# Kernel optimization log

Hardware: AMD Instinct MI355X
Metric: run time of the kernel (lower is better)

The kernel has to match this reference:

```python
import jax, jax.numpy as jnp
import numpy as np

EPS = 1e-5


def setup_inputs() -> dict:
    key = jax.random.key(0)
    k_x, k_y, k_w, k_b = jax.random.split(key, 4)
    B, IN, OUT = 16384, 1024, 1024
    x = jax.random.normal(k_x, (B, IN), dtype=jnp.float32)
    y = jax.random.normal(k_y, (B, OUT), dtype=jnp.float32)
    # nn.Linear default init scale ~ 1/sqrt(in_features); keep activations sane
    weight = jax.random.normal(k_w, (OUT, IN), dtype=jnp.float32) / np.sqrt(IN)
    bias = jax.random.normal(k_b, (OUT,), dtype=jnp.float32) / np.sqrt(IN)
    gamma = jnp.ones((OUT,), dtype=jnp.float32)
    beta = jnp.zeros((OUT,), dtype=jnp.float32)
    return {"x": x, "y": y, "weight": weight, "bias": bias, "gamma": gamma, "beta": beta}


def reference(x, y, weight, bias, gamma, beta):
    # Linear: z[b, o] = sum_i x[b, i] * weight[o, i] + bias[o]
    z = jnp.einsum('bi,oi->bo', x, weight) + bias
    # LayerNorm over the feature (out_features) dim, biased variance
    mean = jnp.mean(z, axis=-1, keepdims=True)
    var = jnp.mean(jnp.square(z), axis=-1, keepdims=True) - jnp.square(mean)
    ln = (z - mean) * jax.lax.rsqrt(var + EPS) * gamma + beta
    # residual add then elementwise multiply
    return (ln + y) * y
```

## Files before the change

kernel.cpp:

```cpp
#include <hip/hip_runtime.h>
#include <stdint.h>

typedef unsigned short u16;
typedef __attribute__((ext_vector_type(8))) short short8;
typedef __attribute__((ext_vector_type(4))) float floatx4;
typedef __attribute__((ext_vector_type(2))) float floatx2;

#define K_DIM 1024
#define N_DIM 1024
#define BM 64
#define BK 32
#define NCHUNK (K_DIM / BK)

__device__ __forceinline__ u16 f2b(float f) {
    union { float f; uint32_t i; } v; v.f = f;
    uint32_t u = v.i;
    return (u16)((u + 0x7FFFu + ((u >> 16) & 1u)) >> 16);
}
__device__ __forceinline__ float b2f(u16 u) {
    union { uint32_t i; float f; } v; v.i = ((uint32_t)u) << 16; return v.f;
}

__global__ __launch_bounds__(256) void pack_w_kernel(const float* __restrict__ w,
                                                     u16* __restrict__ wpk) {
    int gid  = blockIdx.x * 256 + threadIdx.x;
    int lane = gid & 63;
    int kc   = (gid >> 6) & 31;
    int tile = gid >> 11;
    int n = tile * 16 + (lane & 15);
    int k = kc * 32 + (lane >> 4) * 8;
    const float* src = w + (size_t)n * K_DIM + k;
    floatx4 a = *(const floatx4*)(src);
    floatx4 b = *(const floatx4*)(src + 4);
    short8 o;
    o[0] = (short)f2b(a[0]); o[1] = (short)f2b(a[1]);
    o[2] = (short)f2b(a[2]); o[3] = (short)f2b(a[3]);
    o[4] = (short)f2b(b[0]); o[5] = (short)f2b(b[1]);
    o[6] = (short)f2b(b[2]); o[7] = (short)f2b(b[3]);
    *(short8*)(wpk + (size_t)gid * 8) = o;
}

__global__ __launch_bounds__(1024) void fused_gemm_ln_kernel(
    const float* __restrict__ x, const float* __restrict__ y,
    const u16* __restrict__ wpk, const float* __restrict__ bias,
    const float* __restrict__ gamma, const float* __restrict__ beta,
    float* __restrict__ out)
{
    __shared__ __align__(16) u16 lds_a[2][BM * BK];
    __shared__ __align__(16) u16 zbuf[16 * 1024];
    __shared__ float ls_sum[64];
    __shared__ float ls_sum2[64];
    __shared__ float ls_mean[64];
    __shared__ float ls_rs[64];

    const int tid  = threadIdx.x;
    const int lane = tid & 63;
    const int wv   = tid >> 6;
    const int q    = lane >> 4;
    const int row0 = blockIdx.x * BM;

    if (tid < 64) { ls_sum[tid] = 0.0f; ls_sum2[tid] = 0.0f; }

    const int sr = tid >> 4;
    const int sk = (tid & 15) << 1;
    const float* s_src = x + (size_t)(row0 + sr) * K_DIM + sk;
    const int s_qs  = (sk >> 3) ^ ((sr >> 1) & 3);
    const int s_off = sr * 64 + s_qs * 16 + (sk & 7) * 2;

    const u16* bp = wpk + (size_t)wv * 65536 + lane * 8;

    const int a_base = (lane & 15) * 64 + (q ^ (((lane & 15) >> 1) & 3)) * 16;

    floatx4 acc[4][4];
#pragma unroll
    for (int mi = 0; mi < 4; ++mi)
#pragma unroll
        for (int ni = 0; ni < 4; ++ni)
            acc[mi][ni] = (floatx4){0.0f, 0.0f, 0.0f, 0.0f};

    {
        floatx2 v = *(const floatx2*)(s_src);
        uint32_t p = (uint32_t)f2b(v[0]) | ((uint32_t)f2b(v[1]) << 16);
        *(uint32_t*)((char*)(&lds_a[0][0]) + s_off) = p;
    }
    short8 bfr[2][4];
#pragma unroll
    for (int ni = 0; ni < 4; ++ni)
        bfr[0][ni] = *(const short8*)(bp + ni * 16384);

#pragma unroll 2
    for (int kc = 0; kc < NCHUNK; ++kc) {
        const int cur = kc & 1;
        const bool pf = (kc + 1 < NCHUNK);

        __syncthreads();

        short8 afrag[4];
        const char* ab = (const char*)(&lds_a[cur][0]);
#pragma unroll
        for (int mi = 0; mi < 4; ++mi)
            afrag[mi] = *(const short8*)(ab + a_base + mi * 1024);

        floatx2 vn;
        if (pf) {
#pragma unroll
            for (int ni = 0; ni < 4; ++ni)
                bfr[cur ^ 1][ni] = *(const short8*)(bp + ni * 16384 + (kc + 1) * 512);
            vn = *(const floatx2*)(s_src + (kc + 1) * BK);
        }

#pragma unroll
        for (int mi = 0; mi < 4; ++mi)
#pragma unroll
            for (int ni = 0; ni < 4; ++ni)
                acc[mi][ni] = __builtin_amdgcn_mfma_f32_16x16x32_bf16(
                    afrag[mi], bfr[cur][ni], acc[mi][ni], 0, 0, 0);

        if (pf) {
            uint32_t p = (uint32_t)f2b(vn[0]) | ((uint32_t)f2b(vn[1]) << 16);
            *(uint32_t*)((char*)(&lds_a[cur ^ 1][0]) + s_off) = p;
        }
    }

    float bias_v[4];
#pragma unroll
    for (int ni = 0; ni < 4; ++ni)
        bias_v[ni] = bias[(wv << 6) + (ni << 4) + (lane & 15)];
#pragma unroll
    for (int mi = 0; mi < 4; ++mi)
#pragma unroll
        for (int ni = 0; ni < 4; ++ni)
#pragma unroll
            for (int r = 0; r < 4; ++r)
                acc[mi][ni][r] += bias_v[ni];

#pragma unroll
    for (int mi = 0; mi < 4; ++mi)
#pragma unroll
        for (int r = 0; r < 4; ++r) {
            float s = 0.0f, s2 = 0.0f;
#pragma unroll
            for (int ni = 0; ni < 4; ++ni) {
                float v = acc[mi][ni][r];
                s += v; s2 += v * v;
            }
#pragma unroll
            for (int m = 1; m < 16; m <<= 1) {
                s  += __shfl_xor(s,  m, 64);
                s2 += __shfl_xor(s2, m, 64);
            }
            if ((lane & 15) == 0) {
                int rl = (mi << 4) + (q << 2) + r;
                atomicAdd(&ls_sum[rl], s);
                atomicAdd(&ls_sum2[rl], s2);
            }
        }

    __syncthreads();
    if (tid < 64) {
        float mean = ls_sum[tid] * (1.0f / 1024.0f);
        float var  = ls_sum2[tid] * (1.0f / 1024.0f) - mean * mean;
        ls_mean[tid] = mean;
        ls_rs[tid]   = rsqrtf(var + 1e-5f);
    }

    for (int mi = 0; mi < 4; ++mi) {
#pragma unroll
        for (int ni = 0; ni < 4; ++ni)
#pragma unroll
            for (int r = 0; r < 4; ++r) {
                int lr   = (q << 2) + r;
                int lin  = (((wv << 6) + (ni << 4) + (lane & 15)) << 1);
                int phys = lr * 2048 + (lin ^ (q << 5));
                *(u16*)((char*)zbuf + phys) = f2b(acc[mi][ni][r]);
            }
        __syncthreads();
#pragma unroll
        for (int it = 0; it < 2; ++it) {
            int row  = (tid >> 7) + (it << 3);
            int c8   = tid & 127;
            int phys = row * 2048 + ((c8 << 4) ^ (((row >> 2) & 3) << 5));
            short8 z8 = *(const short8*)((const char*)zbuf + phys);
            int grow  = row0 + (mi << 4) + row;
            float mean = ls_mean[(mi << 4) + row];
            float rs   = ls_rs[(mi << 4) + row];
            const float* yp = y     + (size_t)grow * N_DIM + c8 * 8;
            const float* gp = gamma + c8 * 8;
            const float* bpv = beta + c8 * 8;
            float*       op = out   + (size_t)grow * N_DIM + c8 * 8;
            floatx4 y0 = *(const floatx4*)(yp);
            floatx4 y1 = *(const floatx4*)(yp + 4);
            floatx4 g0 = *(const floatx4*)(gp);
            floatx4 g1 = *(const floatx4*)(gp + 4);
            floatx4 b0 = *(const floatx4*)(bpv);
            floatx4 b1 = *(const floatx4*)(bpv + 4);
            floatx4 o0, o1;
#pragma unroll
            for (int e = 0; e < 4; ++e) {
                float zv = b2f((u16)z8[e]);
                o0[e] = ((zv - mean) * rs * g0[e] + b0[e] + y0[e]) * y0[e];
            }
#pragma unroll
            for (int e = 0; e < 4; ++e) {
                float zv = b2f((u16)z8[e + 4]);
                o1[e] = ((zv - mean) * rs * g1[e] + b1[e] + y1[e]) * y1[e];
            }
            *(floatx4*)(op)     = o0;
            *(floatx4*)(op + 4) = o1;
        }
        __syncthreads();
    }
}

extern "C" void kernel_launch(void* const* d_in, const int* in_sizes, int n_in,
                              void* d_out, int out_size, void* d_ws, size_t ws_size,
                              hipStream_t stream) {
    const float* x     = (const float*)d_in[0];
    const float* y     = (const float*)d_in[1];
    const float* wgt   = (const float*)d_in[2];
    const float* bias  = (const float*)d_in[3];
    const float* gamma = (const float*)d_in[4];
    const float* beta  = (const float*)d_in[5];
    float* out = (float*)d_out;
    u16* wpk = (u16*)d_ws;

    pack_w_kernel<<<512, 256, 0, stream>>>(wgt, wpk);

    const int M = in_sizes[0] / K_DIM;
    fused_gemm_ln_kernel<<<M / BM, 1024, 0, stream>>>(x, y, wpk, bias, gamma, beta, out);
}
```

Measured before the change: 227.0 us.

## Halve row tile to 32 and prefetch A two chunks ahead with raw barrier

Shrinks the per-block row tile from 64 to 32, halving accumulator registers and doubling the number of blocks, with launch bounds hinting at higher occupancy. The A-operand load now has each thread fetch one float and prefetch it three chunks ahead in registers, and the per-chunk __syncthreads is replaced by an explicit lgkmcnt wait plus s_barrier. The aim is to hide global latency and raise occupancy. The cost is that every block reloads the full packed weight for only half as many rows, which doubles weight traffic, and the A loads become narrower scalar accesses.

```diff
diff --git a/kernel.cpp b/kernel.cpp
--- a/kernel.cpp
+++ b/kernel.cpp
@@ -8,7 +8,7 @@
 
 #define K_DIM 1024
 #define N_DIM 1024
-#define BM 64
+#define BM 32
 #define BK 32
 #define NCHUNK (K_DIM / BK)
 
@@ -40,7 +40,7 @@
     *(short8*)(wpk + (size_t)gid * 8) = o;
 }
 
-__global__ __launch_bounds__(1024) void fused_gemm_ln_kernel(
+__global__ __launch_bounds__(1024, 8) void fused_gemm_ln_kernel(
     const float* __restrict__ x, const float* __restrict__ y,
     const u16* __restrict__ wpk, const float* __restrict__ bias,
     const float* __restrict__ gamma, const float* __restrict__ beta,
@@ -48,10 +48,10 @@
 {
     __shared__ __align__(16) u16 lds_a[2][BM * BK];
     __shared__ __align__(16) u16 zbuf[16 * 1024];
-    __shared__ float ls_sum[64];
-    __shared__ float ls_sum2[64];
-    __shared__ float ls_mean[64];
-    __shared__ float ls_rs[64];
+    __shared__ float ls_sum[BM];
+    __shared__ float ls_sum2[BM];
+    __shared__ float ls_mean[BM];
+    __shared__ float ls_rs[BM];
 
     const int tid  = threadIdx.x;
     const int lane = tid & 63;
@@ -59,10 +59,10 @@
     const int q    = lane >> 4;
     const int row0 = blockIdx.x * BM;
 
-    if (tid < 64) { ls_sum[tid] = 0.0f; ls_sum2[tid] = 0.0f; }
-
-    const int sr = tid >> 4;
-    const int sk = (tid & 15) << 1;
+    if (tid < BM) { ls_sum[tid] = 0.0f; ls_sum2[tid] = 0.0f; }
+
+    const int sr = tid >> 5;
+    const int sk = tid & 31;
     const float* s_src = x + (size_t)(row0 + sr) * K_DIM + sk;
     const int s_qs  = (sk >> 3) ^ ((sr >> 1) & 3);
     const int s_off = sr * 64 + s_qs * 16 + (sk & 7) * 2;
@@ -71,18 +71,20 @@
 
     const int a_base = (lane & 15) * 64 + (q ^ (((lane & 15) >> 1) & 3)) * 16;
 
-    floatx4 acc[4][4];
-#pragma unroll
-    for (int mi = 0; mi < 4; ++mi)
+    floatx4 acc[2][4];
+#pragma unroll
+    for (int mi = 0; mi < 2; ++mi)
 #pragma unroll
         for (int ni = 0; ni < 4; ++ni)
             acc[mi][ni] = (floatx4){0.0f, 0.0f, 0.0f, 0.0f};
 
     {
-        floatx2 v = *(const floatx2*)(s_src);
-        uint32_t p = (uint32_t)f2b(v[0]) | ((uint32_t)f2b(v[1]) << 16);
-        *(uint32_t*)((char*)(&lds_a[0][0]) + s_off) = p;
-    }
+        float v0 = s_src[0];
+        *(u16*)((char*)(&lds_a[0][0]) + s_off) = f2b(v0);
+    }
+    float va_next = s_src[BK];
+    float va_far  = s_src[2 * BK];
+
     short8 bfr[2][4];
 #pragma unroll
     for (int ni = 0; ni < 4; ++ni)
@@ -91,34 +93,36 @@
 #pragma unroll 2
     for (int kc = 0; kc < NCHUNK; ++kc) {
         const int cur = kc & 1;
-        const bool pf = (kc + 1 < NCHUNK);
-
-        __syncthreads();
-
-        short8 afrag[4];
+        const int nxt = cur ^ 1;
+
+        asm volatile("s_waitcnt lgkmcnt(0)" ::: "memory");
+        __builtin_amdgcn_s_barrier();
+        asm volatile("" ::: "memory");
+
+        short8 afrag[2];
         const char* ab = (const char*)(&lds_a[cur][0]);
-#pragma unroll
-        for (int mi = 0; mi < 4; ++mi)
-            afrag[mi] = *(const short8*)(ab + a_base + mi * 1024);
-
-        floatx2 vn;
-        if (pf) {
+        afrag[0] = *(const short8*)(ab + a_base);
+        afrag[1] = *(const short8*)(ab + a_base + 1024);
+
+        if (kc + 1 < NCHUNK) {
 #pragma unroll
             for (int ni = 0; ni < 4; ++ni)
-                bfr[cur ^ 1][ni] = *(const short8*)(bp + ni * 16384 + (kc + 1) * 512);
-            vn = *(const floatx2*)(s_src + (kc + 1) * BK);
-        }
-
-#pragma unroll
-        for (int mi = 0; mi < 4; ++mi)
+                bfr[nxt][ni] = *(const short8*)(bp + ni * 16384 + (kc + 1) * 512);
+        }
+        float vnew = 0.0f;
+        if (kc + 3 < NCHUNK) vnew = s_src[(kc + 3) * BK];
+
+#pragma unroll
+        for (int mi = 0; mi < 2; ++mi)
 #pragma unroll
             for (int ni = 0; ni < 4; ++ni)
                 acc[mi][ni] = __builtin_amdgcn_mfma_f32_16x16x32_bf16(
                     afrag[mi], bfr[cur][ni], acc[mi][ni], 0, 0, 0);
 
-        if (pf) {
-            uint32_t p = (uint32_t)f2b(vn[0]) | ((uint32_t)f2b(vn[1]) << 16);
-            *(uint32_t*)((char*)(&lds_a[cur ^ 1][0]) + s_off) = p;
+        if (kc + 1 < NCHUNK) {
+            *(u16*)((char*)(&lds_a[nxt][0]) + s_off) = f2b(va_next);
+            va_next = va_far;
+            va_far  = vnew;
         }
     }
 
@@ -127,7 +131,7 @@
     for (int ni = 0; ni < 4; ++ni)
         bias_v[ni] = bias[(wv << 6) + (ni << 4) + (lane & 15)];
 #pragma unroll
-    for (int mi = 0; mi < 4; ++mi)
+    for (int mi = 0; mi < 2; ++mi)
 #pragma unroll
         for (int ni = 0; ni < 4; ++ni)
 #pragma unroll
@@ -135,7 +139,7 @@
                 acc[mi][ni][r] += bias_v[ni];
 
 #pragma unroll
-    for (int mi = 0; mi < 4; ++mi)
+    for (int mi = 0; mi < 2; ++mi)
 #pragma unroll
         for (int r = 0; r < 4; ++r) {
             float s = 0.0f, s2 = 0.0f;
@@ -157,14 +161,14 @@
         }
 
     __syncthreads();
-    if (tid < 64) {
+    if (tid < BM) {
         float mean = ls_sum[tid] * (1.0f / 1024.0f);
         float var  = ls_sum2[tid] * (1.0f / 1024.0f) - mean * mean;
         ls_mean[tid] = mean;
         ls_rs[tid]   = rsqrtf(var + 1e-5f);
     }
 
-    for (int mi = 0; mi < 4; ++mi) {
+    for (int mi = 0; mi < 2; ++mi) {
 #pragma unroll
         for (int ni = 0; ni < 4; ++ni)
 #pragma unroll
```

New measurement: 740.1 us. 226% more time.

## Deepen global prefetch pipeline for A and B fragments in GEMM loop

Applied to the files above, without the earlier changes.

Raises the prefetch distance of the x (A) global loads to three chunks ahead, held in registers, and of the packed-weight (B) fragments to two chunks ahead, so global load latency has more iterations to hide behind MFMA work. The full __syncthreads is replaced by an explicit lgkmcnt(0) wait plus s_barrier, so outstanding global (vmcnt) loads are not drained at every barrier. This costs extra registers for the deeper in-flight buffers and relies on hand-managed wait counts for correctness.

```diff
diff --git a/kernel.cpp b/kernel.cpp
--- a/kernel.cpp
+++ b/kernel.cpp
@@ -79,21 +79,29 @@
             acc[mi][ni] = (floatx4){0.0f, 0.0f, 0.0f, 0.0f};
 
     {
-        floatx2 v = *(const floatx2*)(s_src);
-        uint32_t p = (uint32_t)f2b(v[0]) | ((uint32_t)f2b(v[1]) << 16);
+        floatx2 v0 = *(const floatx2*)(s_src);
+        uint32_t p = (uint32_t)f2b(v0[0]) | ((uint32_t)f2b(v0[1]) << 16);
         *(uint32_t*)((char*)(&lds_a[0][0]) + s_off) = p;
     }
+    floatx2 va_next = *(const floatx2*)(s_src + BK);
+    floatx2 va_far  = *(const floatx2*)(s_src + 2 * BK);
+
     short8 bfr[2][4];
 #pragma unroll
     for (int ni = 0; ni < 4; ++ni)
         bfr[0][ni] = *(const short8*)(bp + ni * 16384);
+#pragma unroll
+    for (int ni = 0; ni < 4; ++ni)
+        bfr[1][ni] = *(const short8*)(bp + ni * 16384 + 512);
 
 #pragma unroll 2
     for (int kc = 0; kc < NCHUNK; ++kc) {
         const int cur = kc & 1;
-        const bool pf = (kc + 1 < NCHUNK);
-
-        __syncthreads();
+        const int nxt = cur ^ 1;
+
+        asm volatile("s_waitcnt lgkmcnt(0)" ::: "memory");
+        __builtin_amdgcn_s_barrier();
+        asm volatile("" ::: "memory");
 
         short8 afrag[4];
         const char* ab = (const char*)(&lds_a[cur][0]);
@@ -101,13 +109,8 @@
         for (int mi = 0; mi < 4; ++mi)
             afrag[mi] = *(const short8*)(ab + a_base + mi * 1024);
 
-        floatx2 vn;
-        if (pf) {
-#pragma unroll
-            for (int ni = 0; ni < 4; ++ni)
-                bfr[cur ^ 1][ni] = *(const short8*)(bp + ni * 16384 + (kc + 1) * 512);
-            vn = *(const floatx2*)(s_src + (kc + 1) * BK);
-        }
+        floatx2 vnew = (floatx2){0.0f, 0.0f};
+        if (kc + 3 < NCHUNK) vnew = *(const floatx2*)(s_src + (kc + 3) * BK);
 
 #pragma unroll
         for (int mi = 0; mi < 4; ++mi)
@@ -116,9 +119,17 @@
                 acc[mi][ni] = __builtin_amdgcn_mfma_f32_16x16x32_bf16(
                     afrag[mi], bfr[cur][ni], acc[mi][ni], 0, 0, 0);
 
-        if (pf) {
-            uint32_t p = (uint32_t)f2b(vn[0]) | ((uint32_t)f2b(vn[1]) << 16);
-            *(uint32_t*)((char*)(&lds_a[cur ^ 1][0]) + s_off) = p;
+        if (kc + 2 < NCHUNK) {
+#pragma unroll
+            for (int ni = 0; ni < 4; ++ni)
+                bfr[cur][ni] = *(const short8*)(bp + ni * 16384 + (kc + 2) * 512);
+        }
+
+        if (kc + 1 < NCHUNK) {
+            uint32_t p = (uint32_t)f2b(va_next[0]) | ((uint32_t)f2b(va_next[1]) << 16);
+            *(uint32_t*)((char*)(&lds_a[nxt][0]) + s_off) = p;
+            va_next = va_far;
+            va_far  = vnew;
         }
     }
 
```

After: 225.2 us. Within noise of the previous version (-0.8%).

## Load A fragments directly from global memory, dropping LDS staging and barriers

Applied to the files above, without the earlier changes.

Each wave now reads its x rows straight from global memory into MFMA A fragments and converts them to bf16 in registers. This replaces the shared LDS double buffer and the per-chunk __syncthreads, removing barrier stalls and LDS traffic. The cost is that all 16 waves redundantly load the same 64 rows of x, roughly 16x more global/L2 reads of x, and the loads are no longer prefetched ahead of use. It also adds a launch-bounds occupancy hint and a barrier before the LDS atomics.

```diff
diff --git a/kernel.cpp b/kernel.cpp
--- a/kernel.cpp
+++ b/kernel.cpp
@@ -40,13 +40,12 @@
     *(short8*)(wpk + (size_t)gid * 8) = o;
 }
 
-__global__ __launch_bounds__(1024) void fused_gemm_ln_kernel(
+__global__ __launch_bounds__(1024, 4) void fused_gemm_ln_kernel(
     const float* __restrict__ x, const float* __restrict__ y,
     const u16* __restrict__ wpk, const float* __restrict__ bias,
     const float* __restrict__ gamma, const float* __restrict__ beta,
     float* __restrict__ out)
 {
-    __shared__ __align__(16) u16 lds_a[2][BM * BK];
     __shared__ __align__(16) u16 zbuf[16 * 1024];
     __shared__ float ls_sum[64];
     __shared__ float ls_sum2[64];
@@ -61,15 +60,9 @@
 
     if (tid < 64) { ls_sum[tid] = 0.0f; ls_sum2[tid] = 0.0f; }
 
-    const int sr = tid >> 4;
-    const int sk = (tid & 15) << 1;
-    const float* s_src = x + (size_t)(row0 + sr) * K_DIM + sk;
-    const int s_qs  = (sk >> 3) ^ ((sr >> 1) & 3);
-    const int s_off = sr * 64 + s_qs * 16 + (sk & 7) * 2;
+    const float* ap = x + (size_t)(row0 + (lane & 15)) * K_DIM + ((lane >> 4) << 3);
 
     const u16* bp = wpk + (size_t)wv * 65536 + lane * 8;
-
-    const int a_base = (lane & 15) * 64 + (q ^ (((lane & 15) >> 1) & 3)) * 16;
 
     floatx4 acc[4][4];
 #pragma unroll
@@ -78,11 +71,6 @@
         for (int ni = 0; ni < 4; ++ni)
             acc[mi][ni] = (floatx4){0.0f, 0.0f, 0.0f, 0.0f};
 
-    {
-        floatx2 v = *(const floatx2*)(s_src);
-        uint32_t p = (uint32_t)f2b(v[0]) | ((uint32_t)f2b(v[1]) << 16);
-        *(uint32_t*)((char*)(&lds_a[0][0]) + s_off) = p;
-    }
     short8 bfr[2][4];
 #pragma unroll
     for (int ni = 0; ni < 4; ++ni)
@@ -91,34 +79,27 @@
 #pragma unroll 2
     for (int kc = 0; kc < NCHUNK; ++kc) {
         const int cur = kc & 1;
-        const bool pf = (kc + 1 < NCHUNK);
-
-        __syncthreads();
-
-        short8 afrag[4];
-        const char* ab = (const char*)(&lds_a[cur][0]);
-#pragma unroll
-        for (int mi = 0; mi < 4; ++mi)
-            afrag[mi] = *(const short8*)(ab + a_base + mi * 1024);
-
-        floatx2 vn;
-        if (pf) {
+
+        if (kc + 1 < NCHUNK) {
 #pragma unroll
             for (int ni = 0; ni < 4; ++ni)
                 bfr[cur ^ 1][ni] = *(const short8*)(bp + ni * 16384 + (kc + 1) * 512);
-            vn = *(const floatx2*)(s_src + (kc + 1) * BK);
-        }
-
-#pragma unroll
-        for (int mi = 0; mi < 4; ++mi)
+        }
+
+#pragma unroll
+        for (int mi = 0; mi < 4; ++mi) {
+            const float* s = ap + (size_t)mi * 16 * K_DIM + kc * BK;
+            floatx4 a0 = *(const floatx4*)(s);
+            floatx4 a1 = *(const floatx4*)(s + 4);
+            short8 af;
+            af[0] = (short)f2b(a0[0]); af[1] = (short)f2b(a0[1]);
+            af[2] = (short)f2b(a0[2]); af[3] = (short)f2b(a0[3]);
+            af[4] = (short)f2b(a1[0]); af[5] = (short)f2b(a1[1]);
+            af[6] = (short)f2b(a1[2]); af[7] = (short)f2b(a1[3]);
 #pragma unroll
             for (int ni = 0; ni < 4; ++ni)
                 acc[mi][ni] = __builtin_amdgcn_mfma_f32_16x16x32_bf16(
-                    afrag[mi], bfr[cur][ni], acc[mi][ni], 0, 0, 0);
-
-        if (pf) {
-            uint32_t p = (uint32_t)f2b(vn[0]) | ((uint32_t)f2b(vn[1]) << 16);
-            *(uint32_t*)((char*)(&lds_a[cur ^ 1][0]) + s_off) = p;
+                    af, bfr[cur][ni], acc[mi][ni], 0, 0, 0);
         }
     }
 
@@ -133,6 +114,8 @@
 #pragma unroll
             for (int r = 0; r < 4; ++r)
                 acc[mi][ni][r] += bias_v[ni];
+
+    __syncthreads();
 
 #pragma unroll
     for (int mi = 0; mi < 4; ++mi)
```

Measured after the change: 301.1 us. +32.6%, slower.
